# Kernel tuning notes

Measured on AMD Instinct MI355X. Metric: run time of the kernel, lower is better.

Reference implementation:

```python
import jax, jax.numpy as jnp
import numpy as np

H = 4  # num_heads


def transformer_conv(x, src, dst, wq, bq, wk, bk, wv, bv, ws, bs):
    # PyG TransformerConv, concat=False, root_weight=True, eval mode (no dropout).
    N = x.shape[0]
    C = wq.shape[1] // H  # per-head channels
    q = (x @ wq + bq).reshape(N, H, C)
    k = (x @ wk + bk).reshape(N, H, C)
    v = (x @ wv + bv).reshape(N, H, C)
    # per-edge attention logits: query at dst, key at src
    logits = (q[dst] * k[src]).sum(-1) / jnp.sqrt(jnp.asarray(C, x.dtype))  # [E,H]
    # scatter-softmax over incoming edges of each destination node
    m = jax.lax.stop_gradient(jax.ops.segment_max(logits, dst, num_segments=N))
    m = jnp.where(jnp.isfinite(m), m, jnp.zeros_like(m))
    e = jnp.exp(logits - m[dst])
    denom = jax.ops.segment_sum(e, dst, num_segments=N)
    alpha = e / (denom[dst] + 1e-16)  # [E,H]
    out = jax.ops.segment_sum(alpha[:, :, None] * v[src], dst, num_segments=N)  # [N,H,C]
    return out.mean(axis=1) + x @ ws + bs  # head-average + skip


def setup_inputs() -> dict:
    key = jax.random.key(0)
    ks = jax.random.split(key, 16)
    N, E, D, HID, OUT = 50000, 800000, 128, 32, 40
    s = 0.05
    inp = {
        "x": jax.random.normal(ks[0], (N, D), jnp.float32),
        "edge_index": jax.random.randint(ks[1], (2, E), 0, N, jnp.int64),
        "wq1": jax.random.normal(ks[2], (D, H * HID), jnp.float32) * s,
        "bq1": jnp.zeros((H * HID,), jnp.float32),
        "wk1": jax.random.normal(ks[3], (D, H * HID), jnp.float32) * s,
        "bk1": jnp.zeros((H * HID,), jnp.float32),
        "wv1": jax.random.normal(ks[4], (D, H * HID), jnp.float32) * s,
        "bv1": jnp.zeros((H * HID,), jnp.float32),
        "ws1": jax.random.normal(ks[5], (D, HID), jnp.float32) * s,
        "bs1": jnp.zeros((HID,), jnp.float32),
        "wq2": jax.random.normal(ks[6], (HID, H * HID), jnp.float32) * s,
        "bq2": jnp.zeros((H * HID,), jnp.float32),
        "wk2": jax.random.normal(ks[7], (HID, H * HID), jnp.float32) * s,
        "bk2": jnp.zeros((H * HID,), jnp.float32),
        "wv2": jax.random.normal(ks[8], (HID, H * HID), jnp.float32) * s,
        "bv2": jnp.zeros((H * HID,), jnp.float32),
        "ws2": jax.random.normal(ks[9], (HID, HID), jnp.float32) * s,
        "bs2": jnp.zeros((HID,), jnp.float32),
        "wc": jax.random.normal(ks[10], (HID, OUT), jnp.float32) * s,
        "bc": jnp.zeros((OUT,), jnp.float32),
    }
    return inp


def reference(x, edge_index, wq1, bq1, wk1, bk1, wv1, bv1, ws1, bs1,
              wq2, bq2, wk2, bk2, wv2, bv2, ws2, bs2, wc, bc):
    src, dst = edge_index[0], edge_index[1]
    h = jax.nn.relu(transformer_conv(x, src, dst, wq1, bq1, wk1, bk1, wv1, bv1, ws1, bs1))
    h = jax.nn.relu(transformer_conv(h, src, dst, wq2, bq2, wk2, bk2, wv2, bv2, ws2, bs2))
    return h @ wc + bc
```

## Files before the change

### kernel.cpp

```cpp
#include <hip/hip_runtime.h>
#include <hip/hip_bf16.h>

typedef __attribute__((ext_vector_type(8))) short short8;
typedef __attribute__((ext_vector_type(4))) float floatx4;
typedef __attribute__((ext_vector_type(4))) unsigned short ushort4v;

__device__ inline unsigned short f2bf(float x) {
    unsigned int u = __float_as_uint(x);
    u += 0x7FFFu + ((u >> 16) & 1u);
    return (unsigned short)(u >> 16);
}
__device__ inline float bf2f(unsigned short h) {
    return __uint_as_float(((unsigned int)h) << 16);
}
__device__ inline float blo(unsigned int u) { return __uint_as_float(u << 16); }
__device__ inline float bhi(unsigned int u) { return __uint_as_float(u & 0xFFFF0000u); }

__global__ __launch_bounds__(256) void hist_kernel(
    const int* __restrict__ dst, int* __restrict__ deg, int E)
{
    int e = blockIdx.x * blockDim.x + threadIdx.x;
    if (e < E) atomicAdd(&deg[dst[e]], 1);
}

__global__ __launch_bounds__(256) void scan_part(
    const int* __restrict__ deg, int* __restrict__ bsum, int N)
{
    __shared__ int ws[4];
    const int base = blockIdx.x * 1024;
    const int tid = threadIdx.x, lane = tid & 63, w = tid >> 6;
    int s = 0;
#pragma unroll
    for (int j = 0; j < 4; j++) {
        int i = base + j * 256 + tid;
        if (i < N) s += deg[i];
    }
#pragma unroll
    for (int off = 1; off < 64; off <<= 1) s += __shfl_xor(s, off, 64);
    if (lane == 0) ws[w] = s;
    __syncthreads();
    if (tid == 0) bsum[blockIdx.x] = ws[0] + ws[1] + ws[2] + ws[3];
}

__global__ __launch_bounds__(64) void scan_tops(
    const int* __restrict__ bsum, int* __restrict__ boff,
    int* __restrict__ rowptr, int nb, int N)
{
    int lane = threadIdx.x;
    int v = (lane < nb) ? bsum[lane] : 0;
    int inc = v;
#pragma unroll
    for (int off = 1; off < 64; off <<= 1) {
        int t = __shfl_up(inc, off, 64);
        if (lane >= off) inc += t;
    }
    if (lane < nb) boff[lane] = inc - v;
    if (lane == 63) rowptr[N] = inc;
}

__global__ __launch_bounds__(256) void scan_final(
    const int* __restrict__ deg, const int* __restrict__ boff,
    int* __restrict__ rowptr, int* __restrict__ cursor, int N)
{
    __shared__ int woff[4];
    const int base = blockIdx.x * 1024;
    const int tid = threadIdx.x, lane = tid & 63, w = tid >> 6;
    const int i0 = base + tid * 4;
    int v0 = (i0     < N) ? deg[i0]     : 0;
    int v1 = (i0 + 1 < N) ? deg[i0 + 1] : 0;
    int v2 = (i0 + 2 < N) ? deg[i0 + 2] : 0;
    int v3 = (i0 + 3 < N) ? deg[i0 + 3] : 0;
    int ts = v0 + v1 + v2 + v3;
    int inc = ts;
#pragma unroll
    for (int off = 1; off < 64; off <<= 1) {
        int t = __shfl_up(inc, off, 64);
        if (lane >= off) inc += t;
    }
    if (lane == 63) woff[w] = inc;
    __syncthreads();
    int wpre = 0;
    if (w > 0) wpre += woff[0];
    if (w > 1) wpre += woff[1];
    if (w > 2) wpre += woff[2];
    int exc = boff[blockIdx.x] + wpre + inc - ts;
    int p0 = exc, p1 = exc + v0, p2 = p1 + v1, p3 = p2 + v2;
    if (i0     < N) { rowptr[i0]     = p0; cursor[i0]     = p0; }
    if (i0 + 1 < N) { rowptr[i0 + 1] = p1; cursor[i0 + 1] = p1; }
    if (i0 + 2 < N) { rowptr[i0 + 2] = p2; cursor[i0 + 2] = p2; }
    if (i0 + 3 < N) { rowptr[i0 + 3] = p3; cursor[i0 + 3] = p3; }
}

__global__ __launch_bounds__(256) void fill_kernel(
    const int* __restrict__ src, const int* __restrict__ dst,
    int* __restrict__ cursor, int* __restrict__ perm, int E)
{
    int e = blockIdx.x * blockDim.x + threadIdx.x;
    if (e >= E) return;
    int pos = atomicAdd(&cursor[dst[e]], 1);
    perm[pos] = src[e];
}

__global__ __launch_bounds__(128) void wprep_all(
    const float* __restrict__ wq1, const float* __restrict__ bq1,
    const float* __restrict__ wk1, const float* __restrict__ bk1,
    const float* __restrict__ wv1, const float* __restrict__ bv1,
    const float* __restrict__ ws1, const float* __restrict__ bs1,
    const float* __restrict__ wq2, const float* __restrict__ bq2,
    const float* __restrict__ wk2, const float* __restrict__ bk2,
    const float* __restrict__ wv2, const float* __restrict__ bv2,
    const float* __restrict__ ws2, const float* __restrict__ bs2,
    unsigned short* __restrict__ wt1h, unsigned short* __restrict__ wt1l,
    float* __restrict__ bias1,
    unsigned short* __restrict__ wt2h, unsigned short* __restrict__ wt2l,
    float* __restrict__ bias2)
{
    const int layer = (blockIdx.x >= 416) ? 1 : 0;
    const int c = blockIdx.x - layer * 416;
    const int t = threadIdx.x;
    const int L = layer ? 32 : 128;
    if (t >= L) return;
    const float* w; const float* b; int cc, ncols;
    if (c < 384) {
        int m = c >> 7; cc = c & 127; ncols = 128;
        if (layer == 0) {
            w = (m == 0) ? wq1 : ((m == 1) ? wk1 : wv1);
            b = (m == 0) ? bq1 : ((m == 1) ? bk1 : bv1);
        } else {
            w = (m == 0) ? wq2 : ((m == 1) ? wk2 : wv2);
            b = (m == 0) ? bq2 : ((m == 1) ? bk2 : bv2);
        }
    } else {
        cc = c - 384; ncols = 32;
        w = layer ? ws2 : ws1; b = layer ? bs2 : bs1;
    }
    unsigned short* wh = layer ? wt2h : wt1h;
    unsigned short* wl = layer ? wt2l : wt1l;
    float* bias = layer ? bias2 : bias1;
    float val = w[t * ncols + cc];
    unsigned short h = f2bf(val);
    wh[c * L + t] = h;
    wl[c * L + t] = f2bf(val - bf2f(h));
    if (t == 0) bias[c] = b[cc];
}

template <int L>
__global__ __launch_bounds__(256) void proj_mfma(
    const float* __restrict__ xin,
    const unsigned short* __restrict__ wt_hi,
    const unsigned short* __restrict__ wt_lo,
    const float* __restrict__ bias,
    float* __restrict__ q, unsigned short* __restrict__ kvp,
    float* __restrict__ skip, int N)
{
    constexpr int LP = L + 8;
    constexpr int KS = L / 32;
    constexpr int SI = (32 * (L / 4)) / 256;
    __shared__ unsigned short xh[2][32 * LP];
    __shared__ unsigned short xl[2][32 * LP];
    __shared__ float scr[4][32 * 36];
    const int tid = threadIdx.x, lane = tid & 63, w = tid >> 6;
    const int li = lane & 15, quad = lane >> 4;
    const int slot = __builtin_amdgcn_readfirstlane(blockIdx.y * 4 + w);
    const bool hasT = slot < 13;

    int t0 = 24, t1 = 25;
    if (slot < 4)       { t0 = slot * 2; t1 = t0 + 1; }
    else if (slot < 12) { t0 = 4 + slot; t1 = 12 + slot; }

    short8 Ah[2][KS], Al[2][KS];
    float bias_r[2][4];
    if (hasT) {
#pragma unroll
        for (int ti = 0; ti < 2; ti++) {
            int tt = ti ? t1 : t0;
#pragma unroll
            for (int ks = 0; ks < KS; ks++) {
                long off = (long)(tt * 16 + li) * L + ks * 32 + quad * 8;
                Ah[ti][ks] = *(const short8*)(wt_hi + off);
                Al[ti][ks] = *(const short8*)(wt_lo + off);
            }
#pragma unroll
            for (int r = 0; r < 4; r++)
                bias_r[ti][r] = bias[tt * 16 + quad * 4 + r];
        }
    }

    const int nb0 = blockIdx.x * 256;
    float* myscr = scr[w];
    unsigned int* su = (unsigned int*)myscr;

    float4 xv[SI];
    auto issue_loads = [&](int c) {
#pragma unroll
        for (int s = 0; s < SI; s++) {
            int f = s * 256 + tid;
            int row = f / (L / 4), c4 = (f - row * (L / 4)) * 4;
            int n = nb0 + c * 32 + row;
            xv[s] = (n < N) ? *(const float4*)(xin + (long)n * L + c4)
                            : make_float4(0.f, 0.f, 0.f, 0.f);
        }
    };
    auto cvt_store = [&](int buf) {
#pragma unroll
        for (int s = 0; s < SI; s++) {
            int f = s * 256 + tid;
            int row = f / (L / 4), c4 = (f - row * (L / 4)) * 4;
            unsigned short h0 = f2bf(xv[s].x), h1 = f2bf(xv[s].y),
                           h2 = f2bf(xv[s].z), h3 = f2bf(xv[s].w);
            ushort4v hs = {h0, h1, h2, h3};
            ushort4v ls = {f2bf(xv[s].x - bf2f(h0)), f2bf(xv[s].y - bf2f(h1)),
                           f2bf(xv[s].z - bf2f(h2)), f2bf(xv[s].w - bf2f(h3))};
            *(ushort4v*)(xh[buf] + row * LP + c4) = hs;
            *(ushort4v*)(xl[buf] + row * LP + c4) = ls;
        }
    };

    issue_loads(0);
    cvt_store(0);
    __syncthreads();

    for (int c = 0; c < 8; c++) {
        if (c < 7) issue_loads(c + 1);
        const int n0c = nb0 + c * 32;
        if (hasT) {
            const int buf = c & 1;
#pragma unroll
            for (int half = 0; half < 2; half++) {
                short8 Bh[KS], Bl[KS];
#pragma unroll
                for (int ks = 0; ks < KS; ks++) {
                    int off = (half * 16 + li) * LP + ks * 32 + quad * 8;
                    Bh[ks] = *(const short8*)(xh[buf] + off);
                    Bl[ks] = *(const short8*)(xl[buf] + off);
                }
                floatx4 accv[2];
#pragma unroll
                for (int ti = 0; ti < 2; ti++) {
                    floatx4 acc = {0.f, 0.f, 0.f, 0.f};
#pragma unroll
                    for (int ks = 0; ks < KS; ks++) {
                        acc = __builtin_amdgcn_mfma_f32_16x16x32_bf16(Ah[ti][ks], Bh[ks], acc, 0, 0, 0);
                        acc = __builtin_amdgcn_mfma_f32_16x16x32_bf16(Ah[ti][ks], Bl[ks], acc, 0, 0, 0);
                        acc = __builtin_amdgcn_mfma_f32_16x16x32_bf16(Al[ti][ks], Bh[ks], acc, 0, 0, 0);
                    }
#pragma unroll
                    for (int r = 0; r < 4; r++) acc[r] += bias_r[ti][r];
                    accv[ti] = acc;
                }
                const int row = half * 16 + li;
                if (slot < 4 || slot == 12) {
                    *(floatx4*)(myscr + row * 36 + quad * 4)      = accv[0];
                    *(floatx4*)(myscr + row * 36 + 16 + quad * 4) = accv[1];
                } else {
                    unsigned int k01 = (unsigned int)f2bf(accv[0][0]) | ((unsigned int)f2bf(accv[0][1]) << 16);
                    unsigned int k23 = (unsigned int)f2bf(accv[0][2]) | ((unsigned int)f2bf(accv[0][3]) << 16);
                    unsigned int v01 = (unsigned int)f2bf(accv[1][0]) | ((unsigned int)f2bf(accv[1][1]) << 16);
                    unsigned int v23 = (unsigned int)f2bf(accv[1][2]) | ((unsigned int)f2bf(accv[1][3]) << 16);
                    uint4 pk = make_uint4(k01, v01, k23, v23);
                    *(uint4*)(su + row * 20 + quad * 4) = pk;
                }
            }
            if (slot < 4) {
#pragma unroll
                for (int it = 0; it < 4; it++) {
                    int idx = it * 64 + lane;
                    int nl = idx >> 3, seg = idx & 7;
                    int node = n0c + nl;
                    if (node < N) {
                        floatx4 vv = *(floatx4*)(myscr + nl * 36 + seg * 4);
                        *(floatx4*)(q + (long)node * 128 + slot * 32 + seg * 4) = vv;
                    }
                }
            } else if (slot == 12) {
#pragma unroll
                for (int it = 0; it < 4; it++) {
                    int idx = it * 64 + lane;
                    int nl = idx >> 3, seg = idx & 7;
                    int node = n0c + nl;
                    if (node < N) {
                        floatx4 vv = *(floatx4*)(myscr + nl * 36 + seg * 4);
                        *(floatx4*)(skip + (long)node * 32 + seg * 4) = vv;
                    }
                }
            } else {
                const int i = slot - 4;
#pragma unroll
                for (int it = 0; it < 2; it++) {
                    int idx = it * 64 + lane;
                    int nl = idx >> 2, part = idx & 3;
                    int node = n0c + nl;
                    if (node < N) {
                        uint4 vv = *(uint4*)(su + nl * 20 + part * 4);
                        *(uint4*)((unsigned int*)(kvp + (long)node * 256) + i * 16 + part * 4) = vv;
                    }
                }
            }
        }
        __syncthreads();
        if (c < 7) cvt_store((c + 1) & 1);
        __syncthreads();
    }
}

template <bool FUSE_CLS>
__global__ __launch_bounds__(256) void attn_kernel(
    const float* __restrict__ q, const unsigned short* __restrict__ kvp,
    const int* __restrict__ rowptr, const int* __restrict__ perm,
    const float* __restrict__ skip, float* __restrict__ h,
    const float* __restrict__ wc, const float* __restrict__ bc,
    float* __restrict__ out, int N, int E)
{
    __shared__ float hrow[4][32];
    const int wid = (blockIdx.x * 256 + threadIdx.x) >> 6;
    const int wv = (threadIdx.x >> 6) & 3;
    const int lane = threadIdx.x & 63;
    if (wid >= N) return;
    const int d = __builtin_amdgcn_readfirstlane(wid);
    const int eh = lane >> 5;
    const int sl = lane & 31;
    const int hh = sl >> 3;
    const int g  = sl & 7;
    const int dimoff = hh * 64 + g * 8;
    const float4 q4 = *(const float4*)(q + (long)d * 128 + hh * 32 + g * 4);
    const int beg = rowptr[d], end = rowptr[d + 1];
    const int n = end - beg;
    const int na = (n + 1) >> 1;
    const int my_off = beg + (eh ? na : 0);
    const int my_cnt = eh ? (n - na) : na;
    const float scale = 0.17677669529663687f;
    float m = -INFINITY, den = 0.f;
    float o0 = 0.f, o1 = 0.f, o2 = 0.f, o3 = 0.f;

    auto eidx = [&](int j) -> int {
        int i = (j < my_cnt) ? (my_off + j) : beg;
        return (i < E) ? i : 0;
    };

    int P0 = perm[eidx(4)], P1 = perm[eidx(5)], P2 = perm[eidx(6)], P3 = perm[eidx(7)];
    uint4 A0, A1, A2, A3;
    {
        int s0 = perm[eidx(0)], s1 = perm[eidx(1)], s2 = perm[eidx(2)], s3 = perm[eidx(3)];
        A0 = *(const uint4*)(kvp + (long)s0 * 256 + dimoff);
        A1 = *(const uint4*)(kvp + (long)s1 * 256 + dimoff);
        A2 = *(const uint4*)(kvp + (long)s2 * 256 + dimoff);
        A3 = *(const uint4*)(kvp + (long)s3 * 256 + dimoff);
    }

    for (int j = 0; j < na; j += 4) {
        uint4 B0 = *(const uint4*)(kvp + (long)P0 * 256 + dimoff);
        uint4 B1 = *(const uint4*)(kvp + (long)P1 * 256 + dimoff);
        uint4 B2 = *(const uint4*)(kvp + (long)P2 * 256 + dimoff);
        uint4 B3 = *(const uint4*)(kvp + (long)P3 * 256 + dimoff);
        int NP0 = perm[eidx(j + 8)],  NP1 = perm[eidx(j + 9)];
        int NP2 = perm[eidx(j + 10)], NP3 = perm[eidx(j + 11)];

        float p0 = q4.x * blo(A0.x) + q4.y * bhi(A0.x) + q4.z * blo(A0.z) + q4.w * bhi(A0.z);
        float p1 = q4.x * blo(A1.x) + q4.y * bhi(A1.x) + q4.z * blo(A1.z) + q4.w * bhi(A1.z);
        float p2 = q4.x * blo(A2.x) + q4.y * bhi(A2.x) + q4.z * blo(A2.z) + q4.w * bhi(A2.z);
        float p3 = q4.x * blo(A3.x) + q4.y * bhi(A3.x) + q4.z * blo(A3.z) + q4.w * bhi(A3.z);
        p0 += __shfl_xor(p0, 1);  p1 += __shfl_xor(p1, 1);  p2 += __shfl_xor(p2, 1);  p3 += __shfl_xor(p3, 1);
        p0 += __shfl_xor(p0, 2);  p1 += __shfl_xor(p1, 2);  p2 += __shfl_xor(p2, 2);  p3 += __shfl_xor(p3, 2);
        p0 += __shfl_xor(p0, 4);  p1 += __shfl_xor(p1, 4);  p2 += __shfl_xor(p2, 4);  p3 += __shfl_xor(p3, 4);
        const float l0 = (j + 0 < my_cnt) ? p0 * scale : -INFINITY;
        const float l1 = (j + 1 < my_cnt) ? p1 * scale : -INFINITY;
        const float l2 = (j + 2 < my_cnt) ? p2 * scale : -INFINITY;
        const float l3 = (j + 3 < my_cnt) ? p3 * scale : -INFINITY;
        const float mb = fmaxf(fmaxf(l0, l1), fmaxf(l2, l3));
        const float nm = fmaxf(fmaxf(m, mb), -1e30f);
        const float sc = __expf(m - nm);
        const float w0 = __expf(l0 - nm), w1 = __expf(l1 - nm);
        const float w2 = __expf(l2 - nm), w3 = __expf(l3 - nm);
        den = den * sc + ((w0 + w1) + (w2 + w3));
        o0 = o0 * sc + w0 * blo(A0.y) + w1 * blo(A1.y) + w2 * blo(A2.y) + w3 * blo(A3.y);
        o1 = o1 * sc + w0 * bhi(A0.y) + w1 * bhi(A1.y) + w2 * bhi(A2.y) + w3 * bhi(A3.y);
        o2 = o2 * sc + w0 * blo(A0.w) + w1 * blo(A1.w) + w2 * blo(A2.w) + w3 * blo(A3.w);
        o3 = o3 * sc + w0 * bhi(A0.w) + w1 * bhi(A1.w) + w2 * bhi(A2.w) + w3 * bhi(A3.w);
        m = nm;
        A0 = B0; A1 = B1; A2 = B2; A3 = B3;
        P0 = NP0; P1 = NP1; P2 = NP2; P3 = NP3;
    }

    {
        const float mo = __shfl_xor(m, 32);
        const float dn = __shfl_xor(den, 32);
        const float b0 = __shfl_xor(o0, 32);
        const float b1 = __shfl_xor(o1, 32);
        const float b2 = __shfl_xor(o2, 32);
        const float b3 = __shfl_xor(o3, 32);
        const float nm = fmaxf(fmaxf(m, mo), -1e30f);
        const float sa = __expf(m - nm);
        const float sb = __expf(mo - nm);
        den = den * sa + dn * sb;
        o0 = o0 * sa + b0 * sb;
        o1 = o1 * sa + b1 * sb;
        o2 = o2 * sa + b2 * sb;
        o3 = o3 * sa + b3 * sb;
    }
    const float inv = 1.f / (den + 1e-16f);
    o0 *= inv; o1 *= inv; o2 *= inv; o3 *= inv;
    o0 += __shfl_xor(o0, 8);  o1 += __shfl_xor(o1, 8);
    o2 += __shfl_xor(o2, 8);  o3 += __shfl_xor(o3, 8);
    o0 += __shfl_xor(o0, 16); o1 += __shfl_xor(o1, 16);
    o2 += __shfl_xor(o2, 16); o3 += __shfl_xor(o3, 16);

    if (lane < 8) {
        float4 sk = *(const float4*)(skip + (long)d * 32 + g * 4);
        float r0 = 0.25f * o0 + sk.x;
        float r1 = 0.25f * o1 + sk.y;
        float r2 = 0.25f * o2 + sk.z;
        float r3 = 0.25f * o3 + sk.w;
        r0 = r0 > 0.f ? r0 : 0.f;
        r1 = r1 > 0.f ? r1 : 0.f;
        r2 = r2 > 0.f ? r2 : 0.f;
        r3 = r3 > 0.f ? r3 : 0.f;
        if (FUSE_CLS) {
            *(float4*)&hrow[wv][g * 4] = make_float4(r0, r1, r2, r3);
        } else {
            *(float4*)(h + (long)d * 32 + g * 4) = make_float4(r0, r1, r2, r3);
        }
    }
    if (FUSE_CLS) {
        __builtin_amdgcn_wave_barrier();
        if (lane < 40) {
            float acc = bc[lane];
#pragma unroll
            for (int l = 0; l < 32; ++l)
                acc = fmaf(hrow[wv][l], wc[l * 40 + lane], acc);
            out[(long)d * 40 + lane] = acc;
        }
    }
}

extern "C" void kernel_launch(void* const* d_in, const int* in_sizes, int n_in,
                              void* d_out, int out_size, void* d_ws, size_t ws_size,
                              hipStream_t stream)
{
    const float* x   = (const float*)d_in[0];
    const int* ei    = (const int*)d_in[1];
    const float* wq1 = (const float*)d_in[2];  const float* bq1 = (const float*)d_in[3];
    const float* wk1 = (const float*)d_in[4];  const float* bk1 = (const float*)d_in[5];
    const float* wv1 = (const float*)d_in[6];  const float* bv1 = (const float*)d_in[7];
    const float* ws1 = (const float*)d_in[8];  const float* bs1 = (const float*)d_in[9];
    const float* wq2 = (const float*)d_in[10]; const float* bq2 = (const float*)d_in[11];
    const float* wk2 = (const float*)d_in[12]; const float* bk2 = (const float*)d_in[13];
    const float* wv2 = (const float*)d_in[14]; const float* bv2 = (const float*)d_in[15];
    const float* ws2 = (const float*)d_in[16]; const float* bs2 = (const float*)d_in[17];
    const float* wc  = (const float*)d_in[18]; const float* bc  = (const float*)d_in[19];

    const int N = in_sizes[0] / 128;
    const int E = in_sizes[1] / 2;
    const int* src = ei;
    const int* dst = ei + E;

    char* p = (char*)d_ws;
    auto take = [&](size_t bytes) { char* r = p; p += (bytes + 255) & ~(size_t)255; return r; };
    float* q             = (float*)take((size_t)N * 128 * 4);
    unsigned short* kvp  = (unsigned short*)take((size_t)N * 256 * 2);
    float* skip          = (float*)take((size_t)N * 32 * 4);
    float* h1            = (float*)take((size_t)N * 32 * 4);
    unsigned short* wt1h = (unsigned short*)take(416 * 128 * 2);
    unsigned short* wt1l = (unsigned short*)take(416 * 128 * 2);
    unsigned short* wt2h = (unsigned short*)take(416 * 32 * 2);
    unsigned short* wt2l = (unsigned short*)take(416 * 32 * 2);
    float* bias1         = (float*)take(416 * 4);
    float* bias2         = (float*)take(416 * 4);
    int* deg             = (int*)take((size_t)N * 4);
    int* rowptr          = (int*)take((size_t)(N + 1) * 4);
    int* cursor          = (int*)take((size_t)N * 4);
    int* perm            = (int*)take((size_t)E * 4);
    int* bsum            = (int*)take(64 * 4);
    int* boff            = (int*)take(64 * 4);

    const dim3 projGrid((N + 255) / 256, 4);
    const int eGrid    = (E + 255) / 256;
    const int attnGrid = (N + 3) / 4;
    const int nb       = (N + 1023) / 1024;

    wprep_all<<<832, 128, 0, stream>>>(wq1, bq1, wk1, bk1, wv1, bv1, ws1, bs1,
                                       wq2, bq2, wk2, bk2, wv2, bv2, ws2, bs2,
                                       wt1h, wt1l, bias1, wt2h, wt2l, bias2);
    hipMemsetAsync(deg, 0, (size_t)N * 4, stream);
    hist_kernel<<<eGrid, 256, 0, stream>>>(dst, deg, E);
    scan_part<<<nb, 256, 0, stream>>>(deg, bsum, N);
    scan_tops<<<1, 64, 0, stream>>>(bsum, boff, rowptr, nb, N);
    scan_final<<<nb, 256, 0, stream>>>(deg, boff, rowptr, cursor, N);
    fill_kernel<<<eGrid, 256, 0, stream>>>(src, dst, cursor, perm, E);

    proj_mfma<128><<<projGrid, 256, 0, stream>>>(x, wt1h, wt1l, bias1, q, kvp, skip, N);
    attn_kernel<false><<<attnGrid, 256, 0, stream>>>(q, kvp, rowptr, perm, skip, h1,
                                                     wc, bc, (float*)d_out, N, E);

    proj_mfma<32><<<projGrid, 256, 0, stream>>>(h1, wt2h, wt2l, bias2, q, kvp, skip, N);
    attn_kernel<true><<<attnGrid, 256, 0, stream>>>(q, kvp, rowptr, perm, skip, h1,
                                                    wc, bc, (float*)d_out, N, E);
}
```

Baseline: 363.4 us.

## Fold softmax scale into Q weights, use exp2, DPP reductions, unmasked main loop

Folds the 1/sqrt(C) attention scale and log2(e) into the query weights and bias during weight packing, so the attention loop can use the hardware exp2 directly with no per-edge scaling. Replaces the LDS-based shuffle reductions with DPP row operations and splits the edge loop into an unmasked main loop plus a masked tail. It also simplifies address arithmetic to 32-bit byte offsets. This cuts per-edge ALU work in the gather-bound attention kernel. The risks are slightly different rounding and reliance on the DPP row_ror/row_bcast semantics being correct.

```diff
diff --git a/kernel.cpp b/kernel.cpp
--- a/kernel.cpp
+++ b/kernel.cpp
@@ -15,6 +15,44 @@
 }
 __device__ inline float blo(unsigned int u) { return __uint_as_float(u << 16); }
 __device__ inline float bhi(unsigned int u) { return __uint_as_float(u & 0xFFFF0000u); }
+
+#if defined(__has_builtin)
+#if __has_builtin(__builtin_amdgcn_exp2f)
+#define EXP2F(x) __builtin_amdgcn_exp2f(x)
+#else
+#define EXP2F(x) exp2f(x)
+#endif
+#if __has_builtin(__builtin_amdgcn_update_dpp)
+#define HAVE_DPP 1
+#endif
+#else
+#define EXP2F(x) exp2f(x)
+#endif
+
+#ifdef HAVE_DPP
+template <int CTRL>
+__device__ __forceinline__ float dppadd(float x) {
+    int s = __builtin_amdgcn_update_dpp(0, __float_as_int(x), CTRL, 0xf, 0xf, true);
+    return x + __int_as_float(s);
+}
+__device__ __forceinline__ float red8(float x) {
+    x = dppadd<0xB1>(x);
+    x = dppadd<0x4E>(x);
+    x = dppadd<0x141>(x);
+    return x;
+}
+__device__ __forceinline__ float xor8add(float x) {
+    return dppadd<0x128>(x);
+}
+#else
+__device__ __forceinline__ float red8(float x) {
+    x += __shfl_xor(x, 1); x += __shfl_xor(x, 2); x += __shfl_xor(x, 4);
+    return x;
+}
+__device__ __forceinline__ float xor8add(float x) { return x + __shfl_xor(x, 8); }
+#endif
+
+template <bool B> struct BC { static constexpr bool value = B; };
 
 __global__ __launch_bounds__(256) void hist_kernel(
     const int* __restrict__ dst, int* __restrict__ deg, int E)
@@ -137,11 +175,13 @@
     unsigned short* wh = layer ? wt2h : wt1h;
     unsigned short* wl = layer ? wt2l : wt1l;
     float* bias = layer ? bias2 : bias1;
-    float val = w[t * ncols + cc];
+    const float QSCL = 0.17677669529663687f * 1.4426950408889634f;
+    const float f = (c < 128) ? QSCL : 1.0f;
+    float val = w[t * ncols + cc] * f;
     unsigned short h = f2bf(val);
     wh[c * L + t] = h;
     wl[c * L + t] = f2bf(val - bf2f(h));
-    if (t == 0) bias[c] = b[cc];
+    if (t == 0) bias[c] = b[cc] * f;
 }
 
 template <int L>
@@ -321,56 +361,53 @@
     const int sl = lane & 31;
     const int hh = sl >> 3;
     const int g  = sl & 7;
-    const int dimoff = hh * 64 + g * 8;
+    const unsigned dby = (unsigned)(hh * 64 + g * 8) * 2u;
+    const char* __restrict__ kvb = (const char*)kvp;
     const float4 q4 = *(const float4*)(q + (long)d * 128 + hh * 32 + g * 4);
     const int beg = rowptr[d], end = rowptr[d + 1];
     const int n = end - beg;
     const int na = (n + 1) >> 1;
+    const int nmin = n - na;
     const int my_off = beg + (eh ? na : 0);
-    const int my_cnt = eh ? (n - na) : na;
-    const float scale = 0.17677669529663687f;
+    const int my_cnt = eh ? nmin : na;
+    const int bsafe = (beg < E) ? beg : (E - 1);
     float m = -INFINITY, den = 0.f;
     float o0 = 0.f, o1 = 0.f, o2 = 0.f, o3 = 0.f;
 
-    auto eidx = [&](int j) -> int {
-        int i = (j < my_cnt) ? (my_off + j) : beg;
-        return (i < E) ? i : 0;
+    auto eidx = [&](int j) -> unsigned {
+        return (unsigned)((j < my_cnt) ? my_off + j : bsafe);
     };
+    auto kvld = [&](int s) -> uint4 {
+        return *(const uint4*)(kvb + ((((unsigned)s) << 9) + dby));
+    };
 
     int P0 = perm[eidx(4)], P1 = perm[eidx(5)], P2 = perm[eidx(6)], P3 = perm[eidx(7)];
-    uint4 A0, A1, A2, A3;
-    {
-        int s0 = perm[eidx(0)], s1 = perm[eidx(1)], s2 = perm[eidx(2)], s3 = perm[eidx(3)];
-        A0 = *(const uint4*)(kvp + (long)s0 * 256 + dimoff);
-        A1 = *(const uint4*)(kvp + (long)s1 * 256 + dimoff);
-        A2 = *(const uint4*)(kvp + (long)s2 * 256 + dimoff);
-        A3 = *(const uint4*)(kvp + (long)s3 * 256 + dimoff);
-    }
-
-    for (int j = 0; j < na; j += 4) {
-        uint4 B0 = *(const uint4*)(kvp + (long)P0 * 256 + dimoff);
-        uint4 B1 = *(const uint4*)(kvp + (long)P1 * 256 + dimoff);
-        uint4 B2 = *(const uint4*)(kvp + (long)P2 * 256 + dimoff);
-        uint4 B3 = *(const uint4*)(kvp + (long)P3 * 256 + dimoff);
-        int NP0 = perm[eidx(j + 8)],  NP1 = perm[eidx(j + 9)];
-        int NP2 = perm[eidx(j + 10)], NP3 = perm[eidx(j + 11)];
+    uint4 A0 = kvld(perm[eidx(0)]), A1 = kvld(perm[eidx(1)]),
+          A2 = kvld(perm[eidx(2)]), A3 = kvld(perm[eidx(3)]);
+
+    int j = 0;
+    auto step = [&](auto mc) {
+        constexpr bool MASKED = decltype(mc)::value;
+        uint4 B0 = kvld(P0), B1 = kvld(P1), B2 = kvld(P2), B3 = kvld(P3);
+        const int NP0 = perm[eidx(j + 8)],  NP1 = perm[eidx(j + 9)];
+        const int NP2 = perm[eidx(j + 10)], NP3 = perm[eidx(j + 11)];
 
         float p0 = q4.x * blo(A0.x) + q4.y * bhi(A0.x) + q4.z * blo(A0.z) + q4.w * bhi(A0.z);
         float p1 = q4.x * blo(A1.x) + q4.y * bhi(A1.x) + q4.z * blo(A1.z) + q4.w * bhi(A1.z);
         float p2 = q4.x * blo(A2.x) + q4.y * bhi(A2.x) + q4.z * blo(A2.z) + q4.w * bhi(A2.z);
         float p3 = q4.x * blo(A3.x) + q4.y * bhi(A3.x) + q4.z * blo(A3.z) + q4.w * bhi(A3.z);
-        p0 += __shfl_xor(p0, 1);  p1 += __shfl_xor(p1, 1);  p2 += __shfl_xor(p2, 1);  p3 += __shfl_xor(p3, 1);
-        p0 += __shfl_xor(p0, 2);  p1 += __shfl_xor(p1, 2);  p2 += __shfl_xor(p2, 2);  p3 += __shfl_xor(p3, 2);
-        p0 += __shfl_xor(p0, 4);  p1 += __shfl_xor(p1, 4);  p2 += __shfl_xor(p2, 4);  p3 += __shfl_xor(p3, 4);
-        const float l0 = (j + 0 < my_cnt) ? p0 * scale : -INFINITY;
-        const float l1 = (j + 1 < my_cnt) ? p1 * scale : -INFINITY;
-        const float l2 = (j + 2 < my_cnt) ? p2 * scale : -INFINITY;
-        const float l3 = (j + 3 < my_cnt) ? p3 * scale : -INFINITY;
-        const float mb = fmaxf(fmaxf(l0, l1), fmaxf(l2, l3));
-        const float nm = fmaxf(fmaxf(m, mb), -1e30f);
-        const float sc = __expf(m - nm);
-        const float w0 = __expf(l0 - nm), w1 = __expf(l1 - nm);
-        const float w2 = __expf(l2 - nm), w3 = __expf(l3 - nm);
+        p0 = red8(p0); p1 = red8(p1); p2 = red8(p2); p3 = red8(p3);
+        if (MASKED) {
+            p0 = (j + 0 < my_cnt) ? p0 : -INFINITY;
+            p1 = (j + 1 < my_cnt) ? p1 : -INFINITY;
+            p2 = (j + 2 < my_cnt) ? p2 : -INFINITY;
+            p3 = (j + 3 < my_cnt) ? p3 : -INFINITY;
+        }
+        const float mb = fmaxf(fmaxf(p0, p1), fmaxf(p2, p3));
+        const float nm = MASKED ? fmaxf(fmaxf(m, mb), -1e30f) : fmaxf(m, mb);
+        const float sc = EXP2F(m - nm);
+        const float w0 = EXP2F(p0 - nm), w1 = EXP2F(p1 - nm);
+        const float w2 = EXP2F(p2 - nm), w3 = EXP2F(p3 - nm);
         den = den * sc + ((w0 + w1) + (w2 + w3));
         o0 = o0 * sc + w0 * blo(A0.y) + w1 * blo(A1.y) + w2 * blo(A2.y) + w3 * blo(A3.y);
         o1 = o1 * sc + w0 * bhi(A0.y) + w1 * bhi(A1.y) + w2 * bhi(A2.y) + w3 * bhi(A3.y);
@@ -379,7 +416,9 @@
         m = nm;
         A0 = B0; A1 = B1; A2 = B2; A3 = B3;
         P0 = NP0; P1 = NP1; P2 = NP2; P3 = NP3;
-    }
+    };
+    for (; j + 4 <= nmin; j += 4) step(BC<false>{});
+    for (; j < na; j += 4)       step(BC<true>{});
 
     {
         const float mo = __shfl_xor(m, 32);
@@ -389,8 +428,8 @@
         const float b2 = __shfl_xor(o2, 32);
         const float b3 = __shfl_xor(o3, 32);
         const float nm = fmaxf(fmaxf(m, mo), -1e30f);
-        const float sa = __expf(m - nm);
-        const float sb = __expf(mo - nm);
+        const float sa = EXP2F(m - nm);
+        const float sb = EXP2F(mo - nm);
         den = den * sa + dn * sb;
         o0 = o0 * sa + b0 * sb;
         o1 = o1 * sa + b1 * sb;
@@ -399,8 +438,8 @@
     }
     const float inv = 1.f / (den + 1e-16f);
     o0 *= inv; o1 *= inv; o2 *= inv; o3 *= inv;
-    o0 += __shfl_xor(o0, 8);  o1 += __shfl_xor(o1, 8);
-    o2 += __shfl_xor(o2, 8);  o3 += __shfl_xor(o3, 8);
+    o0 = xor8add(o0); o1 = xor8add(o1);
+    o2 = xor8add(o2); o3 = xor8add(o3);
     o0 += __shfl_xor(o0, 16); o1 += __shfl_xor(o1, 16);
     o2 += __shfl_xor(o2, 16); o3 += __shfl_xor(o3, 16);
 
```

New measurement: 360.3 us. About the same (-0.8%).
